# Performance work log

Hardware: AMD Instinct MI355X
Metric: run time of the kernel (lower is better)

## Reference

```python
import jax, jax.numpy as jnp
import numpy as np

B, L, D, H = 2, 2048, 1024, 16
DK = D // H  # 64


def setup_inputs() -> dict:
    key = jax.random.key(0)
    ks = jax.random.split(key, 9)
    s = 0.02
    return {
        "x": jax.random.normal(ks[0], (B, L, D), dtype=jnp.float32),
        "wq": jax.random.normal(ks[1], (D, D), dtype=jnp.float32) * s,
        "bq": jax.random.normal(ks[2], (D,), dtype=jnp.float32) * s,
        "wk": jax.random.normal(ks[3], (D, D), dtype=jnp.float32) * s,
        "bk": jax.random.normal(ks[4], (D,), dtype=jnp.float32) * s,
        "wv": jax.random.normal(ks[5], (D, D), dtype=jnp.float32) * s,
        "bv": jax.random.normal(ks[6], (D,), dtype=jnp.float32) * s,
        "wo": jax.random.normal(ks[7], (D, D), dtype=jnp.float32) * s,
        "bo": jax.random.normal(ks[8], (D,), dtype=jnp.float32) * s,
    }


def reference(x, wq, bq, wk, bk, wv, bv, wo, bo):
    b, l, d = x.shape
    # torch nn.Linear: y = x @ W^T + b
    q = (x @ wq.T + bq).reshape(b, l, H, DK).transpose(0, 2, 1, 3)  # (b,h,l,dk)
    k = (x @ wk.T + bk).reshape(b, l, H, DK).transpose(0, 2, 1, 3)
    v = (x @ wv.T + bv).reshape(b, l, H, DK).transpose(0, 2, 1, 3)
    scale = 1.0 / jnp.sqrt(jnp.asarray(DK, dtype=x.dtype))
    scores = jnp.einsum("bhqd,bhkd->bhqk", q, k) * scale  # (b,h,l,l)
    causal = jnp.triu(jnp.ones((l, l), dtype=bool), k=1)  # True above diagonal -> masked
    scores = jnp.where(causal[None, None], -jnp.inf, scores)
    probs = jax.nn.softmax(scores, axis=-1)
    out = jnp.einsum("bhqk,bhkd->bhqd", probs, v)  # (b,h,l,dk)
    out = out.transpose(0, 2, 1, 3).reshape(b, l, d)
    return out @ wo.T + bo
```

## Files before the change

### kernel.cpp

```cpp
#include <hip/hip_runtime.h>
#include <cstdint>

#define SEQ     2048
#define DMODEL  1024
#define NHEAD   16
#define DKH     64
#define NTOK    4096
#define LDQKV   3072

typedef __bf16 bf16x8 __attribute__((ext_vector_type(8)));
typedef __bf16 bf16x4 __attribute__((ext_vector_type(4)));
typedef float  f32x4  __attribute__((ext_vector_type(4)));

#define MFMA_BF16(a, b, c) __builtin_amdgcn_mfma_f32_16x16x32_bf16((a), (b), (c), 0, 0, 0)

#define C2F 0.18033688f

__device__ inline float fast_exp2(float x) {
#if __has_builtin(__builtin_amdgcn_exp2f)
  return __builtin_amdgcn_exp2f(x);
#else
  return __expf(x * 0.69314718056f);
#endif
}

__device__ inline void async_copy16(const void* g, void* l) {
  __builtin_amdgcn_global_load_lds(
      reinterpret_cast<const __attribute__((address_space(1))) void*>(
          reinterpret_cast<uintptr_t>(g)),
      reinterpret_cast<__attribute__((address_space(3))) void*>(
          reinterpret_cast<uintptr_t>(l)),
      16, 0, 0);
}

__device__ inline bf16x4 cvt4(float4 v) {
  bf16x4 r;
  r[0] = (__bf16)v.x; r[1] = (__bf16)v.y; r[2] = (__bf16)v.z; r[3] = (__bf16)v.w;
  return r;
}

__global__ __launch_bounds__(256) void pack_kernel(
    const float4* __restrict__ x,
    const float4* __restrict__ wq, const float4* __restrict__ wk,
    const float4* __restrict__ wv, const float4* __restrict__ wo,
    const float4* __restrict__ bq, const float4* __restrict__ bk,
    const float4* __restrict__ bv,
    bf16x4* __restrict__ xb, bf16x4* __restrict__ wqkv,
    bf16x4* __restrict__ wob, float4* __restrict__ bcat)
{
  const int NX = NTOK * DMODEL / 4;
  const int NW = DMODEL * DMODEL / 4;
  const int TOT = NX + 4 * NW + 3 * (DMODEL / 4);
  for (int g = blockIdx.x * 256 + threadIdx.x; g < TOT; g += gridDim.x * 256) {
    if (g < NX) {
      xb[g] = cvt4(x[g]);
    } else if (g < NX + 3 * NW) {
      int g2 = g - NX;
      const float4* s = (g2 < NW) ? wq : (g2 < 2 * NW ? wk : wv);
      float4 v = s[g2 & (NW - 1)];
      if (g2 < NW) { v.x *= C2F; v.y *= C2F; v.z *= C2F; v.w *= C2F; }
      wqkv[g2] = cvt4(v);
    } else if (g < NX + 4 * NW) {
      int g3 = g - NX - 3 * NW;
      wob[g3] = cvt4(wo[g3]);
    } else {
      int g4 = g - NX - 4 * NW;
      const float4* s = (g4 < 256) ? bq : (g4 < 512 ? bk : bv);
      float4 v = s[g4 & 255];
      if (g4 < 256) { v.x *= C2F; v.y *= C2F; v.z *= C2F; v.w *= C2F; }
      bcat[g4] = v;
    }
  }
}

__global__ __launch_bounds__(512, 2) void gemm_qkv_256(
    const __bf16* __restrict__ A,
    const __bf16* __restrict__ W,
    const float* __restrict__ bias,
    __bf16* __restrict__ C)
{
  constexpr int K = 1024;
  __shared__ __bf16 sA[2][256 * 64];
  __shared__ __bf16 sB[2][256 * 64];
  const int tid  = threadIdx.x;
  const int wave = tid >> 6, lane = tid & 63;
  const int quad = lane >> 4, l16 = lane & 15;
  const int wm = wave >> 2, wn = wave & 3;
  const int swl = l16 & 7;
  const size_t m0 = (size_t)blockIdx.x * 256;
  const size_t n0 = (size_t)blockIdx.y * 256;

  const int srow = lane >> 3;
  const int sgr  = (lane & 7) ^ srow;
  const __bf16* pA = A + (m0 + srow) * K + sgr * 8;
  const __bf16* pB = W + (n0 + srow) * K + sgr * 8;

  f32x4 acc[8][4];
  const f32x4 z = {0.f, 0.f, 0.f, 0.f};
#pragma unroll
  for (int i = 0; i < 8; ++i)
#pragma unroll
    for (int j = 0; j < 4; ++j) acc[i][j] = z;

#define STAGE_QKV(buf, k0)                                                    \
  {                                                                           \
    _Pragma("unroll")                                                         \
    for (int L = 0; L < 4; ++L) {                                             \
      const int c = L * 8 + wave;              \
      async_copy16(pA + (size_t)(c * 8) * K + (k0), &sA[buf][c * 512]);       \
      async_copy16(pB + (size_t)(c * 8) * K + (k0), &sB[buf][c * 512]);       \
    }                                                                         \
  }

  int cur = 0;
  STAGE_QKV(0, 0);
  __syncthreads();

  for (int t = 0; t < 16; ++t) {
    const __bf16* A_ = &sA[cur][0];
    const __bf16* B_ = &sB[cur][0];
    if (t + 1 < 16) STAGE_QKV(cur ^ 1, (t + 1) * 64);

    bf16x8 af[4][2], bw0[2][2], bw1[2][2];
#pragma unroll
    for (int i = 0; i < 4; ++i) {
      const __bf16* r = A_ + (wm * 128 + i * 16 + l16) * 64;
      af[i][0] = *(const bf16x8*)(r + ((quad ^ swl) * 8));
      af[i][1] = *(const bf16x8*)(r + (((4 + quad) ^ swl) * 8));
    }
#pragma unroll
    for (int j = 0; j < 2; ++j) {
      const __bf16* r = B_ + (wn * 64 + j * 16 + l16) * 64;
      bw0[j][0] = *(const bf16x8*)(r + ((quad ^ swl) * 8));
      bw0[j][1] = *(const bf16x8*)(r + (((4 + quad) ^ swl) * 8));
    }
    __builtin_amdgcn_s_setprio(1);
#pragma unroll
    for (int i = 0; i < 4; ++i)
#pragma unroll
      for (int j = 0; j < 2; ++j) {
        acc[i][j] = MFMA_BF16(af[i][0], bw0[j][0], acc[i][j]);
        acc[i][j] = MFMA_BF16(af[i][1], bw0[j][1], acc[i][j]);
      }
    __builtin_amdgcn_s_setprio(0);
    __builtin_amdgcn_s_barrier();

#pragma unroll
    for (int j = 0; j < 2; ++j) {
      const __bf16* r = B_ + (wn * 64 + 32 + j * 16 + l16) * 64;
      bw1[j][0] = *(const bf16x8*)(r + ((quad ^ swl) * 8));
      bw1[j][1] = *(const bf16x8*)(r + (((4 + quad) ^ swl) * 8));
    }
    __builtin_amdgcn_s_setprio(1);
#pragma unroll
    for (int i = 0; i < 4; ++i)
#pragma unroll
      for (int j = 0; j < 2; ++j) {
        acc[i][2 + j] = MFMA_BF16(af[i][0], bw1[j][0], acc[i][2 + j]);
        acc[i][2 + j] = MFMA_BF16(af[i][1], bw1[j][1], acc[i][2 + j]);
      }
    __builtin_amdgcn_s_setprio(0);
    __builtin_amdgcn_s_barrier();

#pragma unroll
    for (int i = 0; i < 4; ++i) {
      const __bf16* r = A_ + (wm * 128 + 64 + i * 16 + l16) * 64;
      af[i][0] = *(const bf16x8*)(r + ((quad ^ swl) * 8));
      af[i][1] = *(const bf16x8*)(r + (((4 + quad) ^ swl) * 8));
    }
    __builtin_amdgcn_s_setprio(1);
#pragma unroll
    for (int i = 0; i < 4; ++i)
#pragma unroll
      for (int j = 0; j < 2; ++j) {
        acc[4 + i][2 + j] = MFMA_BF16(af[i][0], bw1[j][0], acc[4 + i][2 + j]);
        acc[4 + i][2 + j] = MFMA_BF16(af[i][1], bw1[j][1], acc[4 + i][2 + j]);
      }
    __builtin_amdgcn_s_setprio(0);
    __builtin_amdgcn_s_barrier();

    __builtin_amdgcn_s_setprio(1);
#pragma unroll
    for (int i = 0; i < 4; ++i)
#pragma unroll
      for (int j = 0; j < 2; ++j) {
        acc[4 + i][j] = MFMA_BF16(af[i][0], bw0[j][0], acc[4 + i][j]);
        acc[4 + i][j] = MFMA_BF16(af[i][1], bw0[j][1], acc[4 + i][j]);
      }
    __builtin_amdgcn_s_setprio(0);
    asm volatile("s_waitcnt vmcnt(0)" ::: "memory");
    __builtin_amdgcn_s_barrier();
    cur ^= 1;
  }
#undef STAGE_QKV

  float bi[4];
#pragma unroll
  for (int jj = 0; jj < 4; ++jj)
    bi[jj] = bias[n0 + wn * 64 + (jj >> 1) * 32 + (jj & 1) * 16 + l16];

#pragma unroll
  for (int i = 0; i < 8; ++i)
#pragma unroll
    for (int jj = 0; jj < 4; ++jj)
#pragma unroll
      for (int r = 0; r < 4; ++r) {
        size_t row = m0 + wm * 128 + i * 16 + quad * 4 + r;
        size_t col = n0 + wn * 64 + (jj >> 1) * 32 + (jj & 1) * 16 + l16;
        C[row * LDQKV + col] = (__bf16)(acc[i][jj][r] + bi[jj]);
      }
}

template<int BN>
__global__ __launch_bounds__(256) void gemm_bias(
    const __bf16* __restrict__ A, const __bf16* __restrict__ W,
    const float* __restrict__ bias, void* __restrict__ C,
    int ldc, int out_bf16)
{
  constexpr int K = 1024;
  constexpr int JT = BN / 32;
  __shared__ __bf16 sA[2][128 * 32];
  __shared__ __bf16 sB[2][BN * 32];
  const int tid  = threadIdx.x;
  const int wave = tid >> 6, lane = tid & 63;
  const int quad = lane >> 4, l16 = lane & 15;
  const size_t m0 = (size_t)blockIdx.x * 128;
  const size_t n0 = (size_t)blockIdx.y * BN;
  const int wm = (wave & 1) * 64, wn = (wave >> 1) * (BN / 2);

  const int g0 = wave * 2;
  const int sr = lane >> 2;
  const int sc = (lane & 3) * 8;
  const __bf16* pa0 = A + (m0 + g0 * 16 + sr) * K + sc;
  const __bf16* pa1 = pa0 + 16 * K;
  const int brow = (BN == 128) ? g0 * 16 : wave * 16;
  const __bf16* pb0 = W + (n0 + brow + sr) * K + sc;
  const int lo  = g0 * 512;
  const int lob = (BN == 128) ? g0 * 512 : wave * 512;

  f32x4 acc[4][JT];
  const f32x4 z = {0.f, 0.f, 0.f, 0.f};
#pragma unroll
  for (int i = 0; i < 4; ++i)
#pragma unroll
    for (int j = 0; j < JT; ++j) acc[i][j] = z;

  async_copy16(pa0, &sA[0][lo]);
  async_copy16(pa1, &sA[0][lo + 512]);
  async_copy16(pb0, &sB[0][lob]);
  if (BN == 128) async_copy16(pb0 + 16 * K, &sB[0][lob + 512]);

  for (int k0 = 0; k0 < K; k0 += 32) {
    const int cur = (k0 >> 5) & 1, nxt = cur ^ 1;
    __syncthreads();
    if (k0 + 32 < K) {
      async_copy16(pa0 + k0 + 32, &sA[nxt][lo]);
      async_copy16(pa1 + k0 + 32, &sA[nxt][lo + 512]);
      async_copy16(pb0 + k0 + 32, &sB[nxt][lob]);
      if (BN == 128) async_copy16(pb0 + 16 * K + k0 + 32, &sB[nxt][lob + 512]);
    }

    bf16x8 af[4], bw[JT];
#pragma unroll
    for (int i = 0; i < 4; ++i)
      af[i] = *(const bf16x8*)(&sA[cur][(wm + i * 16 + l16) * 32 + quad * 8]);
#pragma unroll
    for (int j = 0; j < JT; ++j)
      bw[j] = *(const bf16x8*)(&sB[cur][(wn + j * 16 + l16) * 32 + quad * 8]);
#pragma unroll
    for (int i = 0; i < 4; ++i)
#pragma unroll
      for (int j = 0; j < JT; ++j)
        acc[i][j] = MFMA_BF16(af[i], bw[j], acc[i][j]);
  }

  float bi[JT];
#pragma unroll
  for (int j = 0; j < JT; ++j) bi[j] = bias[n0 + wn + j * 16 + l16];

#pragma unroll
  for (int i = 0; i < 4; ++i) {
#pragma unroll
    for (int j = 0; j < JT; ++j) {
#pragma unroll
      for (int r = 0; r < 4; ++r) {
        size_t row = m0 + wm + i * 16 + quad * 4 + r;
        size_t col = n0 + wn + j * 16 + l16;
        float v = acc[i][j][r] + bi[j];
        if (out_bf16) ((__bf16*)C)[row * ldc + col] = (__bf16)v;
        else          ((float*)C)[row * ldc + col] = v;
      }
    }
  }
}

__global__ __launch_bounds__(256) void vtrans_kernel(
    const __bf16* __restrict__ qkv, __bf16* __restrict__ vt)
{
  __shared__ __bf16 t[64][66];
  const int tid = threadIdx.x;
  const int bh = blockIdx.x;
  const int b = bh >> 4, h = bh & 15;
  const int l0 = blockIdx.y * 64;
  const int r4 = tid >> 6;
  const int c  = tid & 63;
#pragma unroll
  for (int rep = 0; rep < 16; ++rep) {
    int ll = rep * 4 + r4;
    t[ll][c] = qkv[(size_t)(b * SEQ + l0 + ll) * LDQKV + 2048 + h * DKH + c];
  }
  __syncthreads();
#pragma unroll
  for (int rep = 0; rep < 16; ++rep) {
    int dk = rep * 4 + r4;
    vt[(size_t)(bh * DKH + dk) * SEQ + l0 + c] = t[c][dk];
  }
}

__global__ __launch_bounds__(256) void attn_kernel(
    const __bf16* __restrict__ qkv,
    const __bf16* __restrict__ vt,
    __bf16* __restrict__ attn)
{
  __shared__ __bf16 sK[2][64 * 64];
  __shared__ __bf16 sV[2][64 * 64];
  __shared__ __bf16 pbuf[4][16 * 64];
  const int tid  = threadIdx.x;
  const int wave = tid >> 6, lane = tid & 63;
  const int quad = lane >> 4, l16 = lane & 15;
  const int id = blockIdx.x;
  const int u = (id >> 3) & 31, v = id & 7, w = id >> 8;
  const int bh = v * 4 + w;
  const int ue = u ^ ((w >> 1) << 3);
  const int qb = (w & 1) ? ue : 31 - ue;
  const int b = bh >> 4, h = bh & 15;
  const int q0 = qb * 64;
  const int qw = q0 + wave * 16;
  const size_t tokbase = (size_t)b * SEQ;

  const int srow = lane >> 3;
  const int sgr  = (lane & 7) ^ srow;
  const __bf16* pKsrc = qkv + (tokbase + wave * 16 + srow) * LDQKV + 1024 + h * DKH + sgr * 8;
  const __bf16* pVsrc = vt + ((size_t)bh * DKH + wave * 16 + srow) * SEQ + sgr * 8;
  const int lo = wave * 16 * 64;

  bf16x8 qf[2];
#pragma unroll
  for (int s = 0; s < 2; ++s)
    qf[s] = *(const bf16x8*)(qkv + (tokbase + qw + l16) * LDQKV + h * DKH + s * 32 + quad * 8);

  bf16x8 ones;
#pragma unroll
  for (int i = 0; i < 8; ++i) ones[i] = (__bf16)1.0f;

  f32x4 o[4], lacc;
  const f32x4 z = {0.f, 0.f, 0.f, 0.f};
#pragma unroll
  for (int t = 0; t < 4; ++t) o[t] = z;
  lacc = z;

  __bf16* pb = &pbuf[wave][0];
  const int swl = l16 & 7;

  async_copy16(pKsrc, &sK[0][lo]);
  async_copy16(pKsrc + (size_t)8 * LDQKV, &sK[0][lo + 8 * 64]);
  async_copy16(pVsrc, &sV[0][lo]);
  async_copy16(pVsrc + (size_t)8 * SEQ, &sV[0][lo + 8 * 64]);

  for (int t0 = 0; t0 <= qb; ++t0) {
    const int cur = t0 & 1, nxt = cur ^ 1;
    __syncthreads();
    if (t0 < qb) {
      const size_t koff = (size_t)(t0 + 1) * 64;
      async_copy16(pKsrc + koff * LDQKV, &sK[nxt][lo]);
      async_copy16(pKsrc + (koff + 8) * LDQKV, &sK[nxt][lo + 8 * 64]);
      async_copy16(pVsrc + koff, &sV[nxt][lo]);
      async_copy16(pVsrc + (size_t)8 * SEQ + koff, &sV[nxt][lo + 8 * 64]);
    }
    const __bf16* K_ = &sK[cur][0];
    const __bf16* V_ = &sV[cur][0];

    f32x4 sacc[4];
    __builtin_amdgcn_s_setprio(1);
#pragma unroll
    for (int ct = 0; ct < 4; ++ct) {
      bf16x8 k0 = *(const bf16x8*)(K_ + (ct * 16 + l16) * 64 + ((quad ^ swl) * 8));
      bf16x8 k1 = *(const bf16x8*)(K_ + (ct * 16 + l16) * 64 + (((4 + quad) ^ swl) * 8));
      sacc[ct] = MFMA_BF16(k0, qf[0], z);
      sacc[ct] = MFMA_BF16(k1, qf[1], sacc[ct]);
    }
    __builtin_amdgcn_s_setprio(0);

#pragma unroll
    for (int ct = 0; ct < 4; ++ct) {
      bf16x4 p4;
      if (t0 < qb) {
#pragma unroll
        for (int r = 0; r < 4; ++r) p4[r] = (__bf16)fast_exp2(sacc[ct][r]);
      } else {
#pragma unroll
        for (int r = 0; r < 4; ++r) {
          float sv = (ct * 16 + quad * 4 + r <= wave * 16 + l16) ? sacc[ct][r] : -1e30f;
          p4[r] = (__bf16)fast_exp2(sv);
        }
      }
      *(bf16x4*)(pb + l16 * 64 + (((ct * 4 + quad) ^ (swl << 1)) * 4)) = p4;
    }
    bf16x8 ap0 = *(const bf16x8*)(pb + l16 * 64 + ((quad ^ swl) * 8));
    bf16x8 ap1 = *(const bf16x8*)(pb + l16 * 64 + (((4 + quad) ^ swl) * 8));

    __builtin_amdgcn_s_setprio(1);
    lacc = MFMA_BF16(ap0, ones, lacc);
    lacc = MFMA_BF16(ap1, ones, lacc);

#pragma unroll
    for (int dt = 0; dt < 4; ++dt) {
      bf16x8 v0 = *(const bf16x8*)(V_ + (dt * 16 + l16) * 64 + ((quad ^ swl) * 8));
      bf16x8 v1 = *(const bf16x8*)(V_ + (dt * 16 + l16) * 64 + (((4 + quad) ^ swl) * 8));
      o[dt] = MFMA_BF16(ap0, v0, o[dt]);
      o[dt] = MFMA_BF16(ap1, v1, o[dt]);
    }
    __builtin_amdgcn_s_setprio(0);
  }

  float linv[4];
#pragma unroll
  for (int r = 0; r < 4; ++r) linv[r] = 1.0f / lacc[r];

#pragma unroll
  for (int dt = 0; dt < 4; ++dt)
#pragma unroll
    for (int r = 0; r < 4; ++r)
      attn[(tokbase + qw + quad * 4 + r) * DMODEL + h * DKH + dt * 16 + l16] =
          (__bf16)(o[dt][r] * linv[r]);
}

extern "C" void kernel_launch(void* const* d_in, const int* in_sizes, int n_in,
                              void* d_out, int out_size, void* d_ws, size_t ws_size,
                              hipStream_t stream) {
  const float* x  = (const float*)d_in[0];
  const float* wq = (const float*)d_in[1];
  const float* bq = (const float*)d_in[2];
  const float* wk = (const float*)d_in[3];
  const float* bk = (const float*)d_in[4];
  const float* wv = (const float*)d_in[5];
  const float* bv = (const float*)d_in[6];
  const float* wo = (const float*)d_in[7];
  const float* bo = (const float*)d_in[8];

  char* ws = (char*)d_ws;
  __bf16* xb    = (__bf16*)(ws + 0);
  __bf16* wqkv  = (__bf16*)(ws + 8388608);
  __bf16* wob   = (__bf16*)(ws + 14680064);
  float*  bcat  = (float*)(ws + 16777216);
  __bf16* qkv   = (__bf16*)(ws + 16789504);
  __bf16* vt    = (__bf16*)(ws + 41955328);
  __bf16* attn  = (__bf16*)(ws + 50343936);
  float*  out   = (float*)d_out;

  pack_kernel<<<1024, 256, 0, stream>>>(
      (const float4*)x, (const float4*)wq, (const float4*)wk, (const float4*)wv,
      (const float4*)wo, (const float4*)bq, (const float4*)bk, (const float4*)bv,
      (bf16x4*)xb, (bf16x4*)wqkv, (bf16x4*)wob, (float4*)bcat);

  gemm_qkv_256<<<dim3(16, 12), 512, 0, stream>>>(xb, wqkv, bcat, qkv);

  vtrans_kernel<<<dim3(32, 32), 256, 0, stream>>>(qkv, vt);

  attn_kernel<<<1024, 256, 0, stream>>>(qkv, vt, attn);

  gemm_bias<64><<<dim3(32, 16), 256, 0, stream>>>(attn, wob, bo, out, DMODEL, 0);
}
```

Before: 179.4 us.

## Retile QKV GEMM to 256x192 tiles with XCD-aware block mapping

Changes the QKV projection GEMM tile from 256x256 to 256x192, so the launch grows from 192 to 256 blocks. That fills the 256 CUs and removes the partial wave that left CUs idle. A swizzled block-id mapping groups tiles per XCD so blocks on the same XCD share A/B panels in L2. The inner loop is restructured to load all three B fragments once and run two MFMA phases instead of four, dropping some barriers. In exchange each block does less arithmetic per byte loaded, since the tile is smaller.

```diff
diff --git a/kernel.cpp b/kernel.cpp
--- a/kernel.cpp
+++ b/kernel.cpp
@@ -73,7 +73,7 @@
   }
 }
 
-__global__ __launch_bounds__(512, 2) void gemm_qkv_256(
+__global__ __launch_bounds__(512, 2) void gemm_qkv_256x192(
     const __bf16* __restrict__ A,
     const __bf16* __restrict__ W,
     const float* __restrict__ bias,
@@ -81,33 +81,41 @@
 {
   constexpr int K = 1024;
   __shared__ __bf16 sA[2][256 * 64];
-  __shared__ __bf16 sB[2][256 * 64];
+  __shared__ __bf16 sB[2][192 * 64];
   const int tid  = threadIdx.x;
   const int wave = tid >> 6, lane = tid & 63;
   const int quad = lane >> 4, l16 = lane & 15;
   const int wm = wave >> 2, wn = wave & 3;
   const int swl = l16 & 7;
-  const size_t m0 = (size_t)blockIdx.x * 256;
-  const size_t n0 = (size_t)blockIdx.y * 256;
+  const int bid = blockIdx.x;
+  const int xcd = bid & 7, slot = bid >> 3;
+  const int mt = (xcd >> 1) * 4 + (slot >> 3);
+  const int nt = (xcd & 1) * 8 + (slot & 7);
+  const size_t m0 = (size_t)mt * 256;
+  const size_t n0 = (size_t)nt * 192;
 
   const int srow = lane >> 3;
   const int sgr  = (lane & 7) ^ srow;
   const __bf16* pA = A + (m0 + srow) * K + sgr * 8;
   const __bf16* pB = W + (n0 + srow) * K + sgr * 8;
 
-  f32x4 acc[8][4];
+  f32x4 acc[8][3];
   const f32x4 z = {0.f, 0.f, 0.f, 0.f};
 #pragma unroll
   for (int i = 0; i < 8; ++i)
 #pragma unroll
-    for (int j = 0; j < 4; ++j) acc[i][j] = z;
+    for (int j = 0; j < 3; ++j) acc[i][j] = z;
 
 #define STAGE_QKV(buf, k0)                                                    \
   {                                                                           \
     _Pragma("unroll")                                                         \
-    for (int L = 0; L < 4; ++L) {                                             \
-      const int c = L * 8 + wave;              \
+    for (int L = 0; L < 4; ++L) {                 \
+      const int c = L * 8 + wave;                                             \
       async_copy16(pA + (size_t)(c * 8) * K + (k0), &sA[buf][c * 512]);       \
+    }                                                                         \
+    _Pragma("unroll")                                                         \
+    for (int L = 0; L < 3; ++L) {                 \
+      const int c = L * 8 + wave;                                             \
       async_copy16(pB + (size_t)(c * 8) * K + (k0), &sB[buf][c * 512]);       \
     }                                                                         \
   }
@@ -121,43 +129,26 @@
     const __bf16* B_ = &sB[cur][0];
     if (t + 1 < 16) STAGE_QKV(cur ^ 1, (t + 1) * 64);
 
-    bf16x8 af[4][2], bw0[2][2], bw1[2][2];
+    bf16x8 af[4][2], bw[3][2];
+#pragma unroll
+    for (int j = 0; j < 3; ++j) {
+      const __bf16* r = B_ + (wn * 48 + j * 16 + l16) * 64;
+      bw[j][0] = *(const bf16x8*)(r + ((quad ^ swl) * 8));
+      bw[j][1] = *(const bf16x8*)(r + (((4 + quad) ^ swl) * 8));
+    }
 #pragma unroll
     for (int i = 0; i < 4; ++i) {
       const __bf16* r = A_ + (wm * 128 + i * 16 + l16) * 64;
       af[i][0] = *(const bf16x8*)(r + ((quad ^ swl) * 8));
       af[i][1] = *(const bf16x8*)(r + (((4 + quad) ^ swl) * 8));
     }
-#pragma unroll
-    for (int j = 0; j < 2; ++j) {
-      const __bf16* r = B_ + (wn * 64 + j * 16 + l16) * 64;
-      bw0[j][0] = *(const bf16x8*)(r + ((quad ^ swl) * 8));
-      bw0[j][1] = *(const bf16x8*)(r + (((4 + quad) ^ swl) * 8));
-    }
     __builtin_amdgcn_s_setprio(1);
 #pragma unroll
     for (int i = 0; i < 4; ++i)
 #pragma unroll
-      for (int j = 0; j < 2; ++j) {
-        acc[i][j] = MFMA_BF16(af[i][0], bw0[j][0], acc[i][j]);
-        acc[i][j] = MFMA_BF16(af[i][1], bw0[j][1], acc[i][j]);
-      }
-    __builtin_amdgcn_s_setprio(0);
-    __builtin_amdgcn_s_barrier();
-
-#pragma unroll
-    for (int j = 0; j < 2; ++j) {
-      const __bf16* r = B_ + (wn * 64 + 32 + j * 16 + l16) * 64;
-      bw1[j][0] = *(const bf16x8*)(r + ((quad ^ swl) * 8));
-      bw1[j][1] = *(const bf16x8*)(r + (((4 + quad) ^ swl) * 8));
-    }
-    __builtin_amdgcn_s_setprio(1);
-#pragma unroll
-    for (int i = 0; i < 4; ++i)
-#pragma unroll
-      for (int j = 0; j < 2; ++j) {
-        acc[i][2 + j] = MFMA_BF16(af[i][0], bw1[j][0], acc[i][2 + j]);
-        acc[i][2 + j] = MFMA_BF16(af[i][1], bw1[j][1], acc[i][2 + j]);
+      for (int j = 0; j < 3; ++j) {
+        acc[i][j] = MFMA_BF16(af[i][0], bw[j][0], acc[i][j]);
+        acc[i][j] = MFMA_BF16(af[i][1], bw[j][1], acc[i][j]);
       }
     __builtin_amdgcn_s_setprio(0);
     __builtin_amdgcn_s_barrier();
@@ -172,20 +163,9 @@
 #pragma unroll
     for (int i = 0; i < 4; ++i)
 #pragma unroll
-      for (int j = 0; j < 2; ++j) {
-        acc[4 + i][2 + j] = MFMA_BF16(af[i][0], bw1[j][0], acc[4 + i][2 + j]);
-        acc[4 + i][2 + j] = MFMA_BF16(af[i][1], bw1[j][1], acc[4 + i][2 + j]);
-      }
-    __builtin_amdgcn_s_setprio(0);
-    __builtin_amdgcn_s_barrier();
-
-    __builtin_amdgcn_s_setprio(1);
-#pragma unroll
-    for (int i = 0; i < 4; ++i)
-#pragma unroll
-      for (int j = 0; j < 2; ++j) {
-        acc[4 + i][j] = MFMA_BF16(af[i][0], bw0[j][0], acc[4 + i][j]);
-        acc[4 + i][j] = MFMA_BF16(af[i][1], bw0[j][1], acc[4 + i][j]);
+      for (int j = 0; j < 3; ++j) {
+        acc[4 + i][j] = MFMA_BF16(af[i][0], bw[j][0], acc[4 + i][j]);
+        acc[4 + i][j] = MFMA_BF16(af[i][1], bw[j][1], acc[4 + i][j]);
       }
     __builtin_amdgcn_s_setprio(0);
     asm volatile("s_waitcnt vmcnt(0)" ::: "memory");
@@ -194,20 +174,19 @@
   }
 #undef STAGE_QKV
 
-  float bi[4];
-#pragma unroll
-  for (int jj = 0; jj < 4; ++jj)
-    bi[jj] = bias[n0 + wn * 64 + (jj >> 1) * 32 + (jj & 1) * 16 + l16];
+  float bi[3];
+#pragma unroll
+  for (int j = 0; j < 3; ++j) bi[j] = bias[n0 + wn * 48 + j * 16 + l16];
 
 #pragma unroll
   for (int i = 0; i < 8; ++i)
 #pragma unroll
-    for (int jj = 0; jj < 4; ++jj)
+    for (int j = 0; j < 3; ++j)
 #pragma unroll
       for (int r = 0; r < 4; ++r) {
         size_t row = m0 + wm * 128 + i * 16 + quad * 4 + r;
-        size_t col = n0 + wn * 64 + (jj >> 1) * 32 + (jj & 1) * 16 + l16;
-        C[row * LDQKV + col] = (__bf16)(acc[i][jj][r] + bi[jj]);
+        size_t col = n0 + wn * 48 + j * 16 + l16;
+        C[row * LDQKV + col] = (__bf16)(acc[i][j][r] + bi[j]);
       }
 }
 
@@ -463,7 +442,7 @@
       (const float4*)wo, (const float4*)bq, (const float4*)bk, (const float4*)bv,
       (bf16x4*)xb, (bf16x4*)wqkv, (bf16x4*)wob, (float4*)bcat);
 
-  gemm_qkv_256<<<dim3(16, 12), 512, 0, stream>>>(xb, wqkv, bcat, qkv);
+  gemm_qkv_256x192<<<256, 512, 0, stream>>>(xb, wqkv, bcat, qkv);
 
   vtrans_kernel<<<dim3(32, 32), 256, 0, stream>>>(qkv, vt);
 
```

Result: faster. 175.8 us (-2.1%).
